# Kernel tuning notes

Measured on AMD Instinct MI355X. Metric: run time of the kernel, lower is better.

Reference implementation:

```python
import jax, jax.numpy as jnp
import numpy as np

HIDDEN = 1024   # config.hidden_dim
FF = 4096       # expert MLP hidden (4*hidden)
E = 8           # config.num_experts
K = 2           # config.num_selected_experts (top_k)


def setup_inputs() -> dict:
    key = jax.random.key(0)
    ks = jax.random.split(key, 5)
    s = 0.02
    x = jax.random.normal(ks[0], (2, 2048, HIDDEN), jnp.float32)
    Wr = jax.random.normal(ks[1], (HIDDEN, E), jnp.float32) * s   # router (no bias)
    W1 = jax.random.normal(ks[2], (E, HIDDEN, FF), jnp.float32) * s
    b1 = jnp.zeros((E, FF), jnp.float32)
    W2 = jax.random.normal(ks[3], (E, FF, HIDDEN), jnp.float32) * s
    b2 = jnp.zeros((E, HIDDEN), jnp.float32)
    return {"x": x, "Wr": Wr, "W1": W1, "b1": b1, "W2": W2, "b2": b2}


def reference(x, Wr, W1, b1, W2, b2):
    xs = x.reshape(-1, x.shape[-1])            # [T, H]
    router_logits = xs @ Wr                    # [T, E]
    # softmax_order == 'softmax_topk': softmax over all experts in fp32, then top-k
    all_probs = jax.nn.softmax(router_logits.astype(jnp.float32), axis=-1)
    weights, selected_experts = jax.lax.top_k(all_probs, K)   # [T, K], [T, K]
    T = xs.shape[0]
    # per-token per-expert combine weight (zero where expert not selected)
    combine = jnp.zeros((T, E), jnp.float32).at[
        jnp.arange(T)[:, None], selected_experts
    ].add(weights)                              # [T, E]
    out = jnp.zeros_like(xs)
    for e in range(E):                          # fixed small loop over experts
        h = jax.nn.gelu(xs @ W1[e] + b1[e])     # [T, FF]
        y = h @ W2[e] + b2[e]                   # [T, H]
        out = out + combine[:, e, None].astype(xs.dtype) * y
    return out.reshape(x.shape), router_logits, selected_experts
```

## Files before the change

### kernel.cpp

```cpp
#include <hip/hip_runtime.h>
#include <hip/hip_bf16.h>
#include <stdint.h>

#define HID 1024
#define FFD 4096
#define NE  8
#define NTOK 4096
#define BM 128
#define BN 128
#define BK 32
#define RBCAP 72
#define ROWCAP (RBCAP*BM)

typedef __attribute__((ext_vector_type(8))) short short8;
typedef __attribute__((ext_vector_type(4))) float f32x4;

__device__ __forceinline__ unsigned short f2bf(float f){
  union { float f; unsigned u; } v; v.f = f;
  return (unsigned short)((v.u + 0x7FFFu + ((v.u >> 16) & 1u)) >> 16);
}

__device__ __forceinline__ float gelu_f(float x){
  float u = 0.7978845608028654f * (x + 0.044715f * x * x * x);
  return 0.5f * x * (1.0f + tanhf(u));
}

__device__ __forceinline__ void gload_lds16(const void* g, void* l){
  __builtin_amdgcn_global_load_lds((const __attribute__((address_space(1))) void*)g,
                                   (__attribute__((address_space(3))) void*)l,
                                   16, 0, 0);
}

__global__ __launch_bounds__(256) void router_k(
    const float* __restrict__ x, const float* __restrict__ Wr,
    float* __restrict__ out_logits, float* __restrict__ out_sel,
    int* __restrict__ counts, int* __restrict__ tok_sel, float* __restrict__ tok_w)
{
  const int lane = threadIdx.x & 63;
  const int t = (blockIdx.x << 2) + (threadIdx.x >> 6);
  const float* xr = x + (size_t)t * HID;
  double acc[NE];
  #pragma unroll
  for (int e = 0; e < NE; ++e) acc[e] = 0.0;
  #pragma unroll 4
  for (int h = lane; h < HID; h += 64) {
    float xv = xr[h];
    float4 w0 = *(const float4*)(Wr + (size_t)h * NE);
    float4 w1 = *(const float4*)(Wr + (size_t)h * NE + 4);
    acc[0] += (double)xv * w0.x;  acc[1] += (double)xv * w0.y;
    acc[2] += (double)xv * w0.z;  acc[3] += (double)xv * w0.w;
    acc[4] += (double)xv * w1.x;  acc[5] += (double)xv * w1.y;
    acc[6] += (double)xv * w1.z;  acc[7] += (double)xv * w1.w;
  }
  #pragma unroll
  for (int off = 32; off > 0; off >>= 1) {
    #pragma unroll
    for (int e = 0; e < NE; ++e) acc[e] += __shfl_down(acc[e], off);
  }
  if (lane == 0) {
    float lg[NE], p[NE];
    float mx = -3.4e38f;
    #pragma unroll
    for (int e = 0; e < NE; ++e) { lg[e] = (float)acc[e]; mx = fmaxf(mx, lg[e]); }
    float s = 0.f;
    #pragma unroll
    for (int e = 0; e < NE; ++e) { p[e] = expf(lg[e] - mx); s += p[e]; }
    float inv = 1.0f / s;
    #pragma unroll
    for (int e = 0; e < NE; ++e) p[e] *= inv;
    #pragma unroll
    for (int e = 0; e < NE; ++e) out_logits[(size_t)t * NE + e] = lg[e];
    int e0 = 0;
    #pragma unroll
    for (int e = 1; e < NE; ++e) if (p[e] > p[e0]) e0 = e;
    int e1 = (e0 == 0) ? 1 : 0;
    #pragma unroll
    for (int e = 0; e < NE; ++e) if (e != e0 && p[e] > p[e1]) e1 = e;
    out_sel[(size_t)t * 2 + 0] = (float)e0;
    out_sel[(size_t)t * 2 + 1] = (float)e1;
    tok_sel[t * 2 + 0] = e0;  tok_sel[t * 2 + 1] = e1;
    tok_w[t * 2 + 0] = p[e0]; tok_w[t * 2 + 1] = p[e1];
    atomicAdd(&counts[e0], 1); atomicAdd(&counts[e1], 1);
  }
}

__global__ void scan_k(const int* __restrict__ counts, int* __restrict__ offs,
                       int* __restrict__ rb2e, int* __restrict__ rb2row, int* __restrict__ nrb)
{
  if (threadIdx.x == 0 && blockIdx.x == 0) {
    int row = 0, rb = 0;
    for (int e = 0; e < NE; ++e) {
      offs[e] = row;
      int n = counts[e];
      int nb = (n + BM - 1) / BM;
      for (int b = 0; b < nb; ++b) { rb2e[rb] = e; rb2row[rb] = row + b * BM; rb++; }
      row += nb * BM;
    }
    nrb[0] = rb;
  }
}

__global__ __launch_bounds__(256) void build_k(
    const int* __restrict__ tok_sel, const float* __restrict__ tok_w,
    const int* __restrict__ offs, int* __restrict__ cursors,
    int* __restrict__ pair_tok, float* __restrict__ pair_w)
{
  int t = blockIdx.x * 256 + threadIdx.x;
  #pragma unroll
  for (int j = 0; j < 2; ++j) {
    int e = tok_sel[t * 2 + j];
    int pos = atomicAdd(&cursors[e], 1);
    int p = offs[e] + pos;
    pair_tok[p] = t;
    pair_w[p] = tok_w[t * 2 + j];
  }
}

__global__ __launch_bounds__(256) void gather_k(
    const float* __restrict__ x, const int* __restrict__ pair_tok, unsigned short* __restrict__ Xg)
{
  const int lane = threadIdx.x & 63;
  const int p = (blockIdx.x << 2) + (threadIdx.x >> 6);
  int t = pair_tok[p];
  if (t < 0) return;
  const float* src = x + (size_t)t * HID;
  unsigned short* dst = Xg + (size_t)p * HID;
  #pragma unroll
  for (int i = 0; i < 4; ++i) {
    float4 v = *(const float4*)(src + lane * 4 + i * 256);
    unsigned a = (unsigned)f2bf(v.x) | ((unsigned)f2bf(v.y) << 16);
    unsigned b = (unsigned)f2bf(v.z) | ((unsigned)f2bf(v.w) << 16);
    *(uint2*)(dst + lane * 4 + i * 256) = make_uint2(a, b);
  }
}

template<int KDIM, int NDIM, int LDA, bool DOGELU>
__global__ __launch_bounds__(256) void gemm_k(
    const unsigned short* __restrict__ A, const float* __restrict__ W,
    const float* __restrict__ bias,
    const int* __restrict__ nrb, const int* __restrict__ rb2e, const int* __restrict__ rb2row,
    unsigned short* __restrict__ Hout,
    const int* __restrict__ pair_tok, const float* __restrict__ pair_w,
    float* __restrict__ out)
{
  if ((int)blockIdx.y >= nrb[0]) return;
  const int e    = rb2e[blockIdx.y];
  const int row0 = rb2row[blockIdx.y];
  const int bn   = blockIdx.x * BN;

  __shared__ __align__(16) unsigned short As[BM * BK];
  __shared__ __align__(16) unsigned short Bs[BN * BK];

  const int tid = threadIdx.x;
  const int lane = tid & 63, wave = tid >> 6;
  const int wm = wave >> 1, wn = wave & 1;
  const float* Be = W + (size_t)e * KDIM * NDIM;

  f32x4 acc[4][4];
  #pragma unroll
  for (int m = 0; m < 4; ++m)
    #pragma unroll
    for (int n = 0; n < 4; ++n) acc[m][n] = f32x4{0.f, 0.f, 0.f, 0.f};

  const int bcol = tid & 127;
  const int k0   = (tid >> 7) * 16;

  for (int kt = 0; kt < KDIM; kt += BK) {
    #pragma unroll
    for (int r = 0; r < 2; ++r) {
      int c = r * 256 + tid;
      int arow = c >> 2;
      int koff = (c & 3) * 8;
      const void* gp = (const void*)(A + (size_t)(row0 + arow) * LDA + kt + koff);
      void* lp = (void*)(As + (size_t)(r * 256 + wave * 64) * 8);
      gload_lds16(gp, lp);
    }
    const float* bp = Be + (size_t)(kt + k0) * NDIM + bn + bcol;
    float bv[16];
    #pragma unroll
    for (int k = 0; k < 16; ++k) bv[k] = bp[(size_t)k * NDIM];
    unsigned pk[8];
    #pragma unroll
    for (int k = 0; k < 8; ++k)
      pk[k] = (unsigned)f2bf(bv[2 * k]) | ((unsigned)f2bf(bv[2 * k + 1]) << 16);
    uint4* bd = (uint4*)&Bs[bcol * BK + k0];
    bd[0] = make_uint4(pk[0], pk[1], pk[2], pk[3]);
    bd[1] = make_uint4(pk[4], pk[5], pk[6], pk[7]);

    __syncthreads();

    const int kc = lane >> 4, rsel = lane & 15;
    short8 af[4], bf[4];
    #pragma unroll
    for (int m = 0; m < 4; ++m)
      af[m] = *(const short8*)&As[(wm * 64 + m * 16 + rsel) * BK + kc * 8];
    #pragma unroll
    for (int n = 0; n < 4; ++n)
      bf[n] = *(const short8*)&Bs[(wn * 64 + n * 16 + rsel) * BK + kc * 8];
    #pragma unroll
    for (int m = 0; m < 4; ++m)
      #pragma unroll
      for (int n = 0; n < 4; ++n)
        acc[m][n] = __builtin_amdgcn_mfma_f32_16x16x32_bf16(af[m], bf[n], acc[m][n], 0, 0, 0);

    __syncthreads();
  }

  const int rsel = lane & 15, quad = lane >> 4;
  float bvv[4];
  #pragma unroll
  for (int n = 0; n < 4; ++n)
    bvv[n] = bias[(size_t)e * NDIM + bn + wn * 64 + n * 16 + rsel];

  if constexpr (DOGELU) {
    #pragma unroll
    for (int m = 0; m < 4; ++m) {
      int r0 = row0 + wm * 64 + m * 16 + quad * 4;
      #pragma unroll
      for (int n = 0; n < 4; ++n) {
        int col = bn + wn * 64 + n * 16 + rsel;
        unsigned short* hp = Hout + (size_t)r0 * NDIM + col;
        #pragma unroll
        for (int i = 0; i < 4; ++i) {
          float v = acc[m][n][i] + bvv[n];
          hp[(size_t)i * NDIM] = f2bf(gelu_f(v));
        }
      }
    }
  } else {
    #pragma unroll
    for (int m = 0; m < 4; ++m) {
      #pragma unroll
      for (int i = 0; i < 4; ++i) {
        int p = row0 + wm * 64 + m * 16 + quad * 4 + i;
        int t = pair_tok[p];
        if (t < 0) continue;
        float w = pair_w[p];
        float* op = out + (size_t)t * HID;
        #pragma unroll
        for (int n = 0; n < 4; ++n) {
          int col = bn + wn * 64 + n * 16 + rsel;
          atomicAdd(op + col, w * (acc[m][n][i] + bvv[n]));
        }
      }
    }
  }
}

extern "C" void kernel_launch(void* const* d_in, const int* in_sizes, int n_in,
                              void* d_out, int out_size, void* d_ws, size_t ws_size,
                              hipStream_t stream)
{
  const float* x  = (const float*)d_in[0];
  const float* Wr = (const float*)d_in[1];
  const float* W1 = (const float*)d_in[2];
  const float* b1 = (const float*)d_in[3];
  const float* W2 = (const float*)d_in[4];
  const float* b2 = (const float*)d_in[5];

  float* out        = (float*)d_out;
  float* out_logits = out + (size_t)NTOK * HID;
  float* out_sel    = out_logits + (size_t)NTOK * NE;

  char* ws = (char*)d_ws;
  int*   counts   = (int*)(ws + 0);
  int*   cursors  = (int*)(ws + 64);
  int*   nrb      = (int*)(ws + 128);
  int*   offs     = (int*)(ws + 192);
  int*   rb2e     = (int*)(ws + 256);
  int*   rb2row   = (int*)(ws + 768);
  int*   tok_sel  = (int*)(ws + 1280);
  float* tok_w    = (float*)(ws + 34048);
  int*   pair_tok = (int*)(ws + 66816);
  float* pair_w   = (float*)(ws + 103680);
  unsigned short* Xg = (unsigned short*)(ws + 140800);
  unsigned short* H  = (unsigned short*)(ws + 19015168);

  hipMemsetAsync(ws, 0, 256, stream);
  hipMemsetAsync(pair_tok, 0xFF, (size_t)ROWCAP * 4, stream);
  hipMemsetAsync(d_out, 0, (size_t)out_size * 4, stream);

  router_k<<<NTOK / 4, 256, 0, stream>>>(x, Wr, out_logits, out_sel, counts, tok_sel, tok_w);
  scan_k<<<1, 64, 0, stream>>>(counts, offs, rb2e, rb2row, nrb);
  build_k<<<NTOK / 256, 256, 0, stream>>>(tok_sel, tok_w, offs, cursors, pair_tok, pair_w);
  gather_k<<<ROWCAP / 4, 256, 0, stream>>>(x, pair_tok, Xg);

  dim3 g1(FFD / BN, RBCAP);
  gemm_k<HID, FFD, HID, true><<<g1, 256, 0, stream>>>(
      Xg, W1, b1, nrb, rb2e, rb2row, H, nullptr, nullptr, nullptr);
  dim3 g2(HID / BN, RBCAP);
  gemm_k<FFD, HID, FFD, false><<<g2, 256, 0, stream>>>(
      H, W2, b2, nrb, rb2e, rb2row, nullptr, pair_tok, pair_w, out);
}
```

Measured before the change: 773.3 us.

## Pre-transpose weights to bf16 and split FF dimension into two halves

Adds a transpose kernel that converts W1/W2 slices from fp32 to bf16 in N-major layout, so the GEMM can load B tiles with direct global-to-LDS 16-byte loads instead of strided fp32 loads and in-register conversion. The FF dimension is processed in two halves so the transposed weights and intermediate H fit in the workspace; the second GEMM accumulates into the output per half, adding bias only once. This costs extra kernel launches and a full pass over the weights per call to transpose them.

```diff
diff --git a/kernel.cpp b/kernel.cpp
--- a/kernel.cpp
+++ b/kernel.cpp
@@ -4,6 +4,7 @@
 
 #define HID 1024
 #define FFD 4096
+#define FFH 2048
 #define NE  8
 #define NTOK 4096
 #define BM 128
@@ -134,9 +135,45 @@
   }
 }
 
-template<int KDIM, int NDIM, int LDA, bool DOGELU>
+template<int KSUB, int NSUB>
+__global__ __launch_bounds__(256) void wtrans_k(const float* __restrict__ in,
+                                               unsigned short* __restrict__ out,
+                                               int ld_in, size_t in_estride)
+{
+  const int tilesN = NSUB / 64;
+  const int tk = blockIdx.x / tilesN, tn = blockIdx.x % tilesN;
+  const int k0 = tk * 64, n0 = tn * 64;
+  const float* ine = in + (size_t)blockIdx.y * in_estride;
+  unsigned short* oute = out + (size_t)blockIdx.y * KSUB * NSUB;
+  __shared__ unsigned short lds[64][65];
+  const int t = threadIdx.x;
+  #pragma unroll
+  for (int i = 0; i < 4; ++i) {
+    int f = i * 256 + t;
+    int krow = f >> 4, c4 = (f & 15) * 4;
+    float4 v = *(const float4*)(ine + (size_t)(k0 + krow) * ld_in + n0 + c4);
+    lds[c4 + 0][krow] = f2bf(v.x);
+    lds[c4 + 1][krow] = f2bf(v.y);
+    lds[c4 + 2][krow] = f2bf(v.z);
+    lds[c4 + 3][krow] = f2bf(v.w);
+  }
+  __syncthreads();
+  #pragma unroll
+  for (int i = 0; i < 4; ++i) {
+    int g = i * 256 + t;
+    int nrow = g >> 4, kc = (g & 15) * 4;
+    unsigned short a0 = lds[nrow][kc], a1 = lds[nrow][kc + 1];
+    unsigned short a2 = lds[nrow][kc + 2], a3 = lds[nrow][kc + 3];
+    uint2 w;
+    w.x = (unsigned)a0 | ((unsigned)a1 << 16);
+    w.y = (unsigned)a2 | ((unsigned)a3 << 16);
+    *(uint2*)(oute + (size_t)(n0 + nrow) * KSUB + k0 + kc) = w;
+  }
+}
+
+template<int KDIM, int NDIM, int BIAS_STRIDE, bool DOGELU, bool ADD_BIAS>
 __global__ __launch_bounds__(256) void gemm_k(
-    const unsigned short* __restrict__ A, const float* __restrict__ W,
+    const unsigned short* __restrict__ A, const unsigned short* __restrict__ Bt,
     const float* __restrict__ bias,
     const int* __restrict__ nrb, const int* __restrict__ rb2e, const int* __restrict__ rb2row,
     unsigned short* __restrict__ Hout,
@@ -154,54 +191,42 @@
   const int tid = threadIdx.x;
   const int lane = tid & 63, wave = tid >> 6;
   const int wm = wave >> 1, wn = wave & 1;
-  const float* Be = W + (size_t)e * KDIM * NDIM;
+  const unsigned short* Be = Bt + (size_t)e * KDIM * NDIM;
 
   f32x4 acc[4][4];
   #pragma unroll
   for (int m = 0; m < 4; ++m)
     #pragma unroll
     for (int n = 0; n < 4; ++n) acc[m][n] = f32x4{0.f, 0.f, 0.f, 0.f};
-
-  const int bcol = tid & 127;
-  const int k0   = (tid >> 7) * 16;
 
   for (int kt = 0; kt < KDIM; kt += BK) {
     #pragma unroll
     for (int r = 0; r < 2; ++r) {
       int c = r * 256 + tid;
-      int arow = c >> 2;
+      int mrow = c >> 2;
       int koff = (c & 3) * 8;
-      const void* gp = (const void*)(A + (size_t)(row0 + arow) * LDA + kt + koff);
-      void* lp = (void*)(As + (size_t)(r * 256 + wave * 64) * 8);
-      gload_lds16(gp, lp);
+      const void* gpa = (const void*)(A + (size_t)(row0 + mrow) * KDIM + kt + koff);
+      void* lpa = (void*)(As + (size_t)(r * 256 + wave * 64) * 8);
+      gload_lds16(gpa, lpa);
+      const void* gpb = (const void*)(Be + (size_t)(bn + mrow) * KDIM + kt + koff);
+      void* lpb = (void*)(Bs + (size_t)(r * 256 + wave * 64) * 8);
+      gload_lds16(gpb, lpb);
     }
-    const float* bp = Be + (size_t)(kt + k0) * NDIM + bn + bcol;
-    float bv[16];
-    #pragma unroll
-    for (int k = 0; k < 16; ++k) bv[k] = bp[(size_t)k * NDIM];
-    unsigned pk[8];
-    #pragma unroll
-    for (int k = 0; k < 8; ++k)
-      pk[k] = (unsigned)f2bf(bv[2 * k]) | ((unsigned)f2bf(bv[2 * k + 1]) << 16);
-    uint4* bd = (uint4*)&Bs[bcol * BK + k0];
-    bd[0] = make_uint4(pk[0], pk[1], pk[2], pk[3]);
-    bd[1] = make_uint4(pk[4], pk[5], pk[6], pk[7]);
-
     __syncthreads();
 
-    const int kc = lane >> 4, rsel = lane & 15;
-    short8 af[4], bf[4];
+    const int kc = lane >> 4, rsel0 = lane & 15;
+    short8 af[4], bfr[4];
     #pragma unroll
     for (int m = 0; m < 4; ++m)
-      af[m] = *(const short8*)&As[(wm * 64 + m * 16 + rsel) * BK + kc * 8];
+      af[m] = *(const short8*)&As[(wm * 64 + m * 16 + rsel0) * BK + kc * 8];
     #pragma unroll
     for (int n = 0; n < 4; ++n)
-      bf[n] = *(const short8*)&Bs[(wn * 64 + n * 16 + rsel) * BK + kc * 8];
+      bfr[n] = *(const short8*)&Bs[(wn * 64 + n * 16 + rsel0) * BK + kc * 8];
     #pragma unroll
     for (int m = 0; m < 4; ++m)
       #pragma unroll
       for (int n = 0; n < 4; ++n)
-        acc[m][n] = __builtin_amdgcn_mfma_f32_16x16x32_bf16(af[m], bf[n], acc[m][n], 0, 0, 0);
+        acc[m][n] = __builtin_amdgcn_mfma_f32_16x16x32_bf16(af[m], bfr[n], acc[m][n], 0, 0, 0);
 
     __syncthreads();
   }
@@ -210,7 +235,7 @@
   float bvv[4];
   #pragma unroll
   for (int n = 0; n < 4; ++n)
-    bvv[n] = bias[(size_t)e * NDIM + bn + wn * 64 + n * 16 + rsel];
+    bvv[n] = ADD_BIAS ? bias[(size_t)e * BIAS_STRIDE + bn + wn * 64 + n * 16 + rsel] : 0.f;
 
   if constexpr (DOGELU) {
     #pragma unroll
@@ -273,8 +298,9 @@
   float* tok_w    = (float*)(ws + 34048);
   int*   pair_tok = (int*)(ws + 66816);
   float* pair_w   = (float*)(ws + 103680);
-  unsigned short* Xg = (unsigned short*)(ws + 140800);
-  unsigned short* H  = (unsigned short*)(ws + 19015168);
+  unsigned short* Xg  = (unsigned short*)(ws + 140800);
+  unsigned short* Hh  = (unsigned short*)(ws + 19015168);
+  unsigned short* Wth = (unsigned short*)(ws + 56763904);
 
   hipMemsetAsync(ws, 0, 256, stream);
   hipMemsetAsync(pair_tok, 0xFF, (size_t)ROWCAP * 4, stream);
@@ -285,10 +311,22 @@
   build_k<<<NTOK / 256, 256, 0, stream>>>(tok_sel, tok_w, offs, cursors, pair_tok, pair_w);
   gather_k<<<ROWCAP / 4, 256, 0, stream>>>(x, pair_tok, Xg);
 
-  dim3 g1(FFD / BN, RBCAP);
-  gemm_k<HID, FFD, HID, true><<<g1, 256, 0, stream>>>(
-      Xg, W1, b1, nrb, rb2e, rb2row, H, nullptr, nullptr, nullptr);
-  dim3 g2(HID / BN, RBCAP);
-  gemm_k<FFD, HID, FFD, false><<<g2, 256, 0, stream>>>(
-      H, W2, b2, nrb, rb2e, rb2row, nullptr, pair_tok, pair_w, out);
-}
+  for (int h = 0; h < 2; ++h) {
+    dim3 gt1((HID / 64) * (FFH / 64), NE);
+    wtrans_k<HID, FFH><<<gt1, 256, 0, stream>>>(
+        W1 + (size_t)h * FFH, Wth, FFD, (size_t)HID * FFD);
+    dim3 g1(FFH / BN, RBCAP);
+    gemm_k<HID, FFH, FFD, true, true><<<g1, 256, 0, stream>>>(
+        Xg, Wth, b1 + (size_t)h * FFH, nrb, rb2e, rb2row, Hh, nullptr, nullptr, nullptr);
+    dim3 gt2((FFH / 64) * (HID / 64), NE);
+    wtrans_k<FFH, HID><<<gt2, 256, 0, stream>>>(
+        W2 + (size_t)h * FFH * HID, Wth, HID, (size_t)FFD * HID);
+    dim3 g2(HID / BN, HID / BN == 8 ? RBCAP : RBCAP);
+    if (h == 0)
+      gemm_k<FFH, HID, HID, false, true><<<dim3(HID / BN, RBCAP), 256, 0, stream>>>(
+          Hh, Wth, b2, nrb, rb2e, rb2row, nullptr, pair_tok, pair_w, out);
+    else
+      gemm_k<FFH, HID, HID, false, false><<<dim3(HID / BN, RBCAP), 256, 0, stream>>>(
+          Hh, Wth, b2, nrb, rb2e, rb2row, nullptr, pair_tok, pair_w, out);
+  }
+}
```

Measured after the change: 767.6 us. Within noise of the previous version (-0.7%).
